# Performance work log

Hardware: AMD Instinct MI355X
Metric: run time of the kernel (lower is better)

Reference implementation:

```python
import jax, jax.numpy as jnp
import numpy as np
from jax import lax

IMG_SIZE = 1024.0  # nominal image dimension for generating plausible coords
IOU_THRESHOLD = 0.5


def box_iou(a, b):
    # a: (N,4), b: (M,4) in (x1,y1,x2,y2); returns (N,M) IoU
    area_a = (a[:, 2] - a[:, 0]) * (a[:, 3] - a[:, 1])
    area_b = (b[:, 2] - b[:, 0]) * (b[:, 3] - b[:, 1])
    lt = jnp.maximum(a[:, None, :2], b[None, :, :2])
    rb = jnp.minimum(a[:, None, 2:], b[None, :, 2:])
    wh = jnp.clip(rb - lt, 0.0)
    inter = wh[..., 0] * wh[..., 1]
    return inter / (area_a[:, None] + area_b[None, :] - inter)


def apply_deltas_to_locations(deltas, locations, stride):
    # Faithful to fcos_apply_deltas_to_locations: clip deltas at 0,
    # un-normalize by stride, subtract/add around the center location.
    d = jnp.clip(deltas, 0.0)  # (N,4) = (l, t, r, b)
    xc, yc = locations[:, 0], locations[:, 1]
    x1 = xc - stride * d[:, 0]
    y1 = yc - stride * d[:, 1]
    x2 = xc + stride * d[:, 2]
    y2 = yc + stride * d[:, 3]
    return jnp.stack([x1, y1, x2, y2], axis=1)


def nms_keep(boxes, scores, iou_threshold):
    # Greedy NMS, equivalent to the sequential reference loop:
    # process boxes in decreasing score order; a box survives if it is not
    # suppressed (IoU > thr) by any earlier surviving box.
    n = boxes.shape[0]
    order = jnp.argsort(-scores)  # descending score order
    b = boxes[order]
    iou = box_iou(b, b)  # (N,N), memory-bound pairwise compare
    idx = jnp.arange(n)

    def body(i, keep):
        suppress = (iou[i] > iou_threshold) & (idx > i) & keep[i]
        return keep & ~suppress

    keep_sorted = lax.fori_loop(0, n, body, jnp.ones((n,), dtype=bool))
    # scatter keep mask back to original ordering
    keep_orig = jnp.zeros((n,), dtype=bool).at[order].set(keep_sorted)
    return keep_orig, order, keep_sorted


def setup_inputs() -> dict:
    key = jax.random.key(0)
    k1, k2, k3, k4 = jax.random.split(key, 4)
    N = 8192
    deltas = jax.random.uniform(k1, (N, 4), dtype=jnp.float32) * 8.0  # stride-normalized LTRB
    locations = jax.random.uniform(k2, (N, 2), dtype=jnp.float32) * IMG_SIZE
    scores = jax.random.uniform(k3, (N,), dtype=jnp.float32)
    class_ids = jax.random.randint(k4, (N,), 0, 80, dtype=jnp.int32)
    return {"deltas": deltas, "locations": locations, "scores": scores,
            "class_ids": class_ids, "stride": 8}


def reference(deltas, locations, scores, class_ids, stride):
    # 1) LTRB delta decode (fcos_apply_deltas_to_locations)
    boxes = apply_deltas_to_locations(deltas, locations, stride)
    # 2) class-specific NMS (class_spec_nms): offset boxes per class so that
    #    boxes of different classes never overlap, then run plain NMS.
    max_coordinate = boxes.max()
    offsets = class_ids.astype(boxes.dtype) * (max_coordinate + 1.0)
    boxes_for_nms = boxes + offsets[:, None]
    keep_orig, order, keep_sorted = nms_keep(boxes_for_nms, scores, IOU_THRESHOLD)
    # boxes: decoded boxes; keep_orig: NMS survival mask (original order);
    # order: score-descending permutation (kept indices = order[keep_sorted])
    return boxes, keep_orig, order
```

## Files before the change

kernel.cpp:

```cpp
#include <hip/hip_runtime.h>

typedef unsigned long long u64;
typedef unsigned int u32;

#define NBOX 8192
#define NW64 128
#define NCLASS 80
#define NCMAX 256
#define CHKCAP 256
#define NS 32
#define SLICE 256
#define NBLK 32
#define RANKB (NS * NBLK)
#define K2GRID (RANKB + 1 + NCLASS)
#define K3GRID (NBLK + 1)

__device__ __forceinline__ u32 f32_mono(float f) {
  u32 u = __float_as_uint(f);
  return (u & 0x80000000u) ? ~u : (u | 0x80000000u);
}
__device__ __forceinline__ float mono_f32(u32 u) {
  u32 b = (u & 0x80000000u) ? (u ^ 0x80000000u) : ~u;
  return __uint_as_float(b);
}
__device__ __forceinline__ u64 readlane64(u64 v, int l) {
  u32 lo = __builtin_amdgcn_readlane((u32)v, l);
  u32 hi = __builtin_amdgcn_readlane((u32)(v >> 32), l);
  return ((u64)hi << 32) | (u64)lo;
}
__device__ __forceinline__ u32 reduce_bmax(const u32* __restrict__ bmax, int t) {
  u32 bm = bmax[t & 31];
#pragma unroll
  for (int off = 16; off > 0; off >>= 1) {
    u32 o = __shfl_xor(bm, off);
    bm = (bm > o) ? bm : o;
  }
  return bm;
}


__global__ __launch_bounds__(256) void decode_kernel(
    const float4* __restrict__ deltas, const float2* __restrict__ locs,
    const int* __restrict__ stride_p, float4* __restrict__ boxes_out,
    u32* __restrict__ bmax) {
  const int t = threadIdx.x;
  const int i = blockIdx.x * 256 + t;
  __shared__ u32 wmax[4];
  float s = (float)(*stride_p);
  float4 d = deltas[i];
  d.x = fmaxf(d.x, 0.f); d.y = fmaxf(d.y, 0.f);
  d.z = fmaxf(d.z, 0.f); d.w = fmaxf(d.w, 0.f);
  float2 c = locs[i];
  float4 bb;
  bb.x = c.x - s * d.x;
  bb.y = c.y - s * d.y;
  bb.z = c.x + s * d.z;
  bb.w = c.y + s * d.w;
  boxes_out[i] = bb;
  float m = fmaxf(fmaxf(bb.x, bb.y), fmaxf(bb.z, bb.w));
  u32 u = f32_mono(m);
#pragma unroll
  for (int off = 32; off > 0; off >>= 1) {
    u32 o = __shfl_xor(u, off);
    u = (u > o) ? u : o;
  }
  if ((t & 63) == 0) wmax[t >> 6] = u;
  __syncthreads();
  if (t == 0) {
    u32 m0 = wmax[0] > wmax[1] ? wmax[0] : wmax[1];
    u32 m1 = wmax[2] > wmax[3] ? wmax[2] : wmax[3];
    bmax[blockIdx.x] = m0 > m1 ? m0 : m1;
  }
}

__global__ __launch_bounds__(256) void rank_nms_kernel(
    const float* __restrict__ scores, const int* __restrict__ class_ids,
    const float4* __restrict__ boxes, const u32* __restrict__ bmax,
    float* __restrict__ keep_out, int* __restrict__ flag,
    int* __restrict__ rankp) {
  const int t = threadIdx.x;
  const int b = blockIdx.x;

  if (b < RANKB) {
    const int bi = b & 31;
    const int slice = b >> 5;
    const int i = bi * 256 + t;
    __shared__ u32 st[SLICE];
    st[t] = f32_mono(scores[slice * 256 + t]);
    __syncthreads();
    u32 mi = f32_mono(scores[i]);
    int tp = i - slice * 256;
    int cnt = 0;
#pragma unroll 8
    for (int p = 0; p < SLICE; ++p) {
      u32 mj = st[p];
      bool less = (mj > mi) || (mj == mi && p < tp);
      cnt += less ? 1 : 0;
    }
    rankp[slice * NBOX + i] = cnt;
    return;
  }

  if (b == RANKB) {
    __shared__ float4 bxA[CHKCAP], bxB[CHKCAP];
    __shared__ int clsA[CHKCAP], clsB[CHKCAP];
    __shared__ int hist[NCLASS];
    __shared__ int na, nb, hitf;
    if (t == 0) { na = 0; nb = 0; hitf = 0; }
    if (t < NCLASS) hist[t] = 0;
    __syncthreads();
    float M = mono_f32(reduce_bmax(bmax, t));
    float thrA = M - 65.0f;
    for (int base = 0; base < NBOX; base += 256) {
      int i = base + t;
      float4 bb = boxes[i];
      int cls = class_ids[i];
      atomicAdd(&hist[cls], 1);
      if (bb.z > thrA && bb.w > thrA) {
        int p = atomicAdd(&na, 1);
        if (p < CHKCAP) { bxA[p] = bb; clsA[p] = cls; }
      }
      if (bb.x < 1.0f && bb.y < 1.0f) {
        int p = atomicAdd(&nb, 1);
        if (p < CHKCAP) { bxB[p] = bb; clsB[p] = cls; }
      }
    }
    __syncthreads();
    if (t < NCLASS && hist[t] > NCMAX) atomicOr(&hitf, 1);
    int NA = na < CHKCAP ? na : CHKCAP;
    int NB = nb < CHKCAP ? nb : CHKCAP;
    bool hit = (t == 0) && (na > CHKCAP || nb > CHKCAP);
    for (int pr = t; pr < NA * NB; pr += 256) {
      int a = pr / NB, b2 = pr % NB;
      if (clsB[b2] != clsA[a] + 1) continue;
      float offa = (float)clsA[a] * (M + 1.0f);
      float offb = (float)clsB[b2] * (M + 1.0f);
      float4 A = bxA[a], Bb = bxB[b2];
      A.x += offa; A.y += offa; A.z += offa; A.w += offa;
      Bb.x += offb; Bb.y += offb; Bb.z += offb; Bb.w += offb;
      float ltx = fmaxf(A.x, Bb.x), lty = fmaxf(A.y, Bb.y);
      float rbx = fminf(A.z, Bb.z), rby = fminf(A.w, Bb.w);
      float ww = fmaxf(rbx - ltx, 0.f), hh = fmaxf(rby - lty, 0.f);
      float inter = ww * hh;
      float aa = (A.z - A.x) * (A.w - A.y);
      float ab = (Bb.z - Bb.x) * (Bb.w - Bb.y);
      float iou = inter / (aa + ab - inter);
      if (iou > 0.4f) hit = true;
    }
    if (hit) atomicOr(&hitf, 1);
    __syncthreads();
    if (t == 0) *flag = hitf;
    return;
  }

  const int c = b - (RANKB + 1);
  __shared__ u64 ck[NCMAX];
  __shared__ u32 slist[NCMAX];
  __shared__ float4 bx[NCMAX];
  __shared__ u64 smask[NCMAX][4];
  __shared__ int cnt_s;
  if (t == 0) cnt_s = 0;
  __syncthreads();

  float M = mono_f32(reduce_bmax(bmax, t));
  float off = (float)c * (M + 1.0f);

  {
    const int4* ci4 = (const int4*)class_ids;
    const float4* sc4 = (const float4*)scores;
#pragma unroll
    for (int it = 0; it < 8; ++it) {
      int g = it * 256 + t;
      int4 c4 = ci4[g];
      float4 s4 = sc4[g];
      int e = g * 4;
      if (c4.x == c) { int p = atomicAdd(&cnt_s, 1); if (p < NCMAX) ck[p] = ((u64)(~f32_mono(s4.x)) << 32) | (u32)(e); }
      if (c4.y == c) { int p = atomicAdd(&cnt_s, 1); if (p < NCMAX) ck[p] = ((u64)(~f32_mono(s4.y)) << 32) | (u32)(e + 1); }
      if (c4.z == c) { int p = atomicAdd(&cnt_s, 1); if (p < NCMAX) ck[p] = ((u64)(~f32_mono(s4.z)) << 32) | (u32)(e + 2); }
      if (c4.w == c) { int p = atomicAdd(&cnt_s, 1); if (p < NCMAX) ck[p] = ((u64)(~f32_mono(s4.w)) << 32) | (u32)(e + 3); }
    }
  }
  __syncthreads();
  int nc = cnt_s;
  if (nc > NCMAX) return;

  if (t < nc) {
    u64 kme = ck[t];
    int r2 = 0;
    for (int p = 0; p < nc; ++p) r2 += (ck[p] < kme) ? 1 : 0;
    slist[r2] = (u32)kme;
  }
  __syncthreads();

  for (int k = t; k < nc; k += 256) {
    float4 bb = boxes[slist[k]];
    bb.x += off; bb.y += off; bb.z += off; bb.w += off;
    bx[k] = bb;
  }
  __syncthreads();

  {
    const int wv = t >> 6;
    const int lane = t & 63;
    const int nw = (nc + 63) >> 6;
    for (int i = wv; i < nc; i += 4) {
      float4 bi = bx[i];
      float area_i = (bi.z - bi.x) * (bi.w - bi.y);
      for (int w = 0; w < nw; ++w) {
        int j2 = w * 64 + lane;
        float4 bj = bx[j2 < NCMAX ? j2 : 0];
        float ltx = fmaxf(bi.x, bj.x), lty = fmaxf(bi.y, bj.y);
        float rbx = fminf(bi.z, bj.z), rby = fminf(bi.w, bj.w);
        float ww = fmaxf(rbx - ltx, 0.f), hh = fmaxf(rby - lty, 0.f);
        float inter = ww * hh;
        float area_j = (bj.z - bj.x) * (bj.w - bj.y);
        float iou = inter / (area_i + area_j - inter);
        bool p = (iou > 0.5f) && (j2 > i) && (j2 < nc);
        u64 mm = __ballot(p);
        if (lane == 0) smask[i][w] = mm;
      }
    }
  }
  __syncthreads();
  if (t >= 64) return;

  u64 ma[4], mb[4], mc[4], md[4];
#pragma unroll
  for (int w = 0; w < 4; ++w) {
    ma[w] = smask[t][w];
    mb[w] = smask[64 + t][w];
    mc[w] = smask[128 + t][w];
    md[w] = smask[192 + t][w];
  }
  u64 R0 = 0, R1 = 0, R2 = 0, R3 = 0;
  u64 K0 = 0, K1 = 0, K2 = 0, K3 = 0;

#define SCAND(D, MD, RD, KD)                                                   \
  {                                                                            \
    int lim = nc - (D) * 64;                                                   \
    if (lim > 0) {                                                             \
      if (lim > 64) lim = 64;                                                  \
      for (int ii = 0; ii < lim; ++ii) {                                       \
        u64 kb = ((RD >> ii) & 1ull) ^ 1ull;                                   \
        KD |= kb << ii;                                                        \
        u64 sm2 = 0ull - kb;                                                   \
        R0 |= readlane64(MD[0], ii) & sm2;                                     \
        R1 |= readlane64(MD[1], ii) & sm2;                                     \
        R2 |= readlane64(MD[2], ii) & sm2;                                     \
        R3 |= readlane64(MD[3], ii) & sm2;                                     \
      }                                                                        \
    }                                                                          \
  }
  SCAND(0, ma, R0, K0)
  SCAND(1, mb, R1, K1)
  SCAND(2, mc, R2, K2)
  SCAND(3, md, R3, K3)
#undef SCAND

  u64 kk[4] = {K0, K1, K2, K3};
#pragma unroll
  for (int d = 0; d < 4; ++d) {
    int j = d * 64 + t;
    if (j < nc) keep_out[slist[j]] = ((kk[d] >> t) & 1ull) ? 1.0f : 0.0f;
  }
}

__global__ __launch_bounds__(256) void scatter_fallback_kernel(
    const int* __restrict__ class_ids, const float4* __restrict__ boxes,
    const u32* __restrict__ bmax, const int* __restrict__ rankp,
    float* __restrict__ order_out, float* __restrict__ keep_out,
    const int* __restrict__ flag) {
  const int t = threadIdx.x;
  const int bid = blockIdx.x;

  if (bid < NBLK) {
    int i = bid * 256 + t;
    int r = 0;
#pragma unroll
    for (int s2 = 0; s2 < NS; ++s2) r += rankp[s2 * NBOX + i];
    order_out[r] = (float)i;
    return;
  }

  if (*flag == 0) return;
  __shared__ u32 perm[NBOX];
  __shared__ u64 remv[NW64];
  for (int k = t; k < NW64; k += 256) remv[k] = 0;
  for (int i = t; i < NBOX; i += 256) {
    int r = 0;
#pragma unroll
    for (int s2 = 0; s2 < NS; ++s2) r += rankp[s2 * NBOX + i];
    perm[r] = (u32)i;
  }
  __syncthreads();
  float maxc = mono_f32(reduce_bmax(bmax, t));
  if (t < 64) {
    int lane = t;
    for (int ii = 0; ii < NBOX; ++ii) {
      if ((remv[ii >> 6] >> (ii & 63)) & 1ull) continue;
      u32 pi = perm[ii];
      float offi = (float)class_ids[pi] * (maxc + 1.0f);
      float4 bi = boxes[pi];
      bi.x += offi; bi.y += offi; bi.z += offi; bi.w += offi;
      float area_i = (bi.z - bi.x) * (bi.w - bi.y);
      for (int jb = ii + 1; jb < NBOX; jb += 64) {
        int j = jb + lane;
        bool p = false;
        if (j < NBOX) {
          u32 pj = perm[j];
          float offj = (float)class_ids[pj] * (maxc + 1.0f);
          float4 bj = boxes[pj];
          bj.x += offj; bj.y += offj; bj.z += offj; bj.w += offj;
          float ltx = fmaxf(bi.x, bj.x), lty = fmaxf(bi.y, bj.y);
          float rbx = fminf(bi.z, bj.z), rby = fminf(bi.w, bj.w);
          float ww = fmaxf(rbx - ltx, 0.f), hh = fmaxf(rby - lty, 0.f);
          float inter = ww * hh;
          float area_j = (bj.z - bj.x) * (bj.w - bj.y);
          float iou = inter / (area_i + area_j - inter);
          p = iou > 0.5f;
        }
        u64 m = __ballot(p);
        if (lane == 0 && m) {
          int w0 = jb >> 6, sh = jb & 63;
          remv[w0] |= (m << sh);
          if (sh && (w0 + 1) < NW64) remv[w0 + 1] |= (m >> (64 - sh));
        }
      }
    }
  }
  __syncthreads();
  for (int k = t; k < NBOX; k += 256)
    keep_out[perm[k]] = ((remv[k >> 6] >> (k & 63)) & 1ull) ? 0.0f : 1.0f;
}

extern "C" void kernel_launch(void* const* d_in, const int* in_sizes, int n_in,
                              void* d_out, int out_size, void* d_ws, size_t ws_size,
                              hipStream_t stream) {
  const float* deltas = (const float*)d_in[0];
  const float* locs = (const float*)d_in[1];
  const float* scores = (const float*)d_in[2];
  const int* class_ids = (const int*)d_in[3];
  const int* stride_p = (const int*)d_in[4];

  float* boxes_out = (float*)d_out;
  float* keep_out = (float*)d_out + (size_t)NBOX * 4;
  float* order_out = (float*)d_out + (size_t)NBOX * 5;

  u32* bmax = (u32*)((char*)d_ws + 64);
  int* flag = (int*)((char*)d_ws + 256);
  int* rankp = (int*)((char*)d_ws + 4096);

  decode_kernel<<<NBLK, 256, 0, stream>>>(
      (const float4*)deltas, (const float2*)locs, stride_p,
      (float4*)boxes_out, bmax);

  rank_nms_kernel<<<K2GRID, 256, 0, stream>>>(
      scores, class_ids, (const float4*)boxes_out, bmax, keep_out, flag,
      rankp);

  scatter_fallback_kernel<<<K3GRID, 256, 0, stream>>>(
      class_ids, (const float4*)boxes_out, bmax, rankp, order_out, keep_out,
      flag);
}
```

Baseline: 45.64 us.

## Reorder fused kernel blocks, union shared memory, move class histogram into decode

```diff
diff --git a/kernel.cpp b/kernel.cpp
--- a/kernel.cpp
+++ b/kernel.cpp
@@ -12,8 +12,9 @@
 #define SLICE 256
 #define NBLK 32
 #define RANKB (NS * NBLK)
-#define K2GRID (RANKB + 1 + NCLASS)
+#define K2GRID (NCLASS + 1 + RANKB)
 #define K3GRID (NBLK + 1)
+#define SMEMSZ 15616
 
 __device__ __forceinline__ u32 f32_mono(float f) {
   u32 u = __float_as_uint(f);
@@ -41,11 +42,14 @@
 
 __global__ __launch_bounds__(256) void decode_kernel(
     const float4* __restrict__ deltas, const float2* __restrict__ locs,
-    const int* __restrict__ stride_p, float4* __restrict__ boxes_out,
-    u32* __restrict__ bmax) {
+    const int* __restrict__ stride_p, const int* __restrict__ class_ids,
+    float4* __restrict__ boxes_out, u32* __restrict__ bmax,
+    int* __restrict__ ccpart) {
   const int t = threadIdx.x;
   const int i = blockIdx.x * 256 + t;
   __shared__ u32 wmax[4];
+  __shared__ int lhist[NCLASS];
+  if (t < NCLASS) lhist[t] = 0;
   float s = (float)(*stride_p);
   float4 d = deltas[i];
   d.x = fmaxf(d.x, 0.f); d.y = fmaxf(d.y, 0.f);
@@ -66,67 +70,177 @@
   }
   if ((t & 63) == 0) wmax[t >> 6] = u;
   __syncthreads();
+  atomicAdd(&lhist[class_ids[i]], 1);
   if (t == 0) {
     u32 m0 = wmax[0] > wmax[1] ? wmax[0] : wmax[1];
     u32 m1 = wmax[2] > wmax[3] ? wmax[2] : wmax[3];
     bmax[blockIdx.x] = m0 > m1 ? m0 : m1;
   }
+  __syncthreads();
+  if (t < NCLASS) ccpart[blockIdx.x * NCLASS + t] = lhist[t];
 }
 
 __global__ __launch_bounds__(256) void rank_nms_kernel(
     const float* __restrict__ scores, const int* __restrict__ class_ids,
     const float4* __restrict__ boxes, const u32* __restrict__ bmax,
-    float* __restrict__ keep_out, int* __restrict__ flag,
-    int* __restrict__ rankp) {
+    const int* __restrict__ ccpart, float* __restrict__ keep_out,
+    int* __restrict__ flag, int* __restrict__ rankp) {
   const int t = threadIdx.x;
-  const int b = blockIdx.x;
-
-  if (b < RANKB) {
-    const int bi = b & 31;
-    const int slice = b >> 5;
-    const int i = bi * 256 + t;
-    __shared__ u32 st[SLICE];
-    st[t] = f32_mono(scores[slice * 256 + t]);
-    __syncthreads();
-    u32 mi = f32_mono(scores[i]);
-    int tp = i - slice * 256;
-    int cnt = 0;
+  const int bid = blockIdx.x;
+  __shared__ __align__(16) char smem[SMEMSZ];
+
+  if (bid < NCLASS) {
+    const int c = bid;
+    u64* ck = (u64*)smem;
+    u32* slist = (u32*)(smem + 2048);
+    float4* bx = (float4*)(smem + 3072);
+    u64(*smask)[4] = (u64(*)[4])(smem + 7168);
+    int* cnt_s = (int*)(smem + 15360);
+    if (t == 0) *cnt_s = 0;
+    __syncthreads();
+
+    float M = mono_f32(reduce_bmax(bmax, t));
+    float off = (float)c * (M + 1.0f);
+
+    {
+      const int4* ci4 = (const int4*)class_ids;
+      const float4* sc4 = (const float4*)scores;
+#pragma unroll
+      for (int it = 0; it < 8; ++it) {
+        int g = it * 256 + t;
+        int4 c4 = ci4[g];
+        float4 s4 = sc4[g];
+        int e = g * 4;
+        if (c4.x == c) { int p = atomicAdd(cnt_s, 1); if (p < NCMAX) ck[p] = ((u64)(~f32_mono(s4.x)) << 32) | (u32)(e); }
+        if (c4.y == c) { int p = atomicAdd(cnt_s, 1); if (p < NCMAX) ck[p] = ((u64)(~f32_mono(s4.y)) << 32) | (u32)(e + 1); }
+        if (c4.z == c) { int p = atomicAdd(cnt_s, 1); if (p < NCMAX) ck[p] = ((u64)(~f32_mono(s4.z)) << 32) | (u32)(e + 2); }
+        if (c4.w == c) { int p = atomicAdd(cnt_s, 1); if (p < NCMAX) ck[p] = ((u64)(~f32_mono(s4.w)) << 32) | (u32)(e + 3); }
+      }
+    }
+    __syncthreads();
+    int nc = *cnt_s;
+    if (nc > NCMAX) return;
+
+    if (t < nc) {
+      u64 kme = ck[t];
+      int r2 = 0;
+      for (int p = 0; p < nc; ++p) r2 += (ck[p] < kme) ? 1 : 0;
+      slist[r2] = (u32)kme;
+    }
+    __syncthreads();
+
+    for (int k = t; k < nc; k += 256) {
+      float4 bb = boxes[slist[k]];
+      bb.x += off; bb.y += off; bb.z += off; bb.w += off;
+      bx[k] = bb;
+    }
+    __syncthreads();
+
+    {
+      const int wv = t >> 6;
+      const int lane = t & 63;
+      const int nw = (nc + 63) >> 6;
+      for (int i = wv; i < nc; i += 4) {
+        float4 bi = bx[i];
+        float area_i = (bi.z - bi.x) * (bi.w - bi.y);
+        for (int w = 0; w < nw; ++w) {
+          int j2 = w * 64 + lane;
+          float4 bj = bx[j2 < NCMAX ? j2 : 0];
+          float ltx = fmaxf(bi.x, bj.x), lty = fmaxf(bi.y, bj.y);
+          float rbx = fminf(bi.z, bj.z), rby = fminf(bi.w, bj.w);
+          float ww = fmaxf(rbx - ltx, 0.f), hh = fmaxf(rby - lty, 0.f);
+          float inter = ww * hh;
+          float area_j = (bj.z - bj.x) * (bj.w - bj.y);
+          float iou = inter / (area_i + area_j - inter);
+          bool p = (iou > 0.5f) && (j2 > i) && (j2 < nc);
+          u64 mm = __ballot(p);
+          if (lane == 0) smask[i][w] = mm;
+        }
+      }
+    }
+    __syncthreads();
+    if (t >= 64) return;
+
+    u64 ma[4], mb[4], mc[4], md[4];
+#pragma unroll
+    for (int w = 0; w < 4; ++w) {
+      ma[w] = smask[t][w];
+      mb[w] = smask[64 + t][w];
+      mc[w] = smask[128 + t][w];
+      md[w] = smask[192 + t][w];
+    }
+    u64 R0 = 0, R1 = 0, R2 = 0, R3 = 0;
+    u64 K0 = 0, K1 = 0, K2 = 0, K3 = 0;
+
+#define SCAND(D, MD, RD, KD)                                                   \
+  {                                                                            \
+    int lim = nc - (D) * 64;                                                   \
+    if (lim > 0) {                                                             \
+      if (lim > 64) lim = 64;                                                  \
+      for (int ii = 0; ii < lim; ++ii) {                                       \
+        u64 kb = ((RD >> ii) & 1ull) ^ 1ull;                                   \
+        KD |= kb << ii;                                                        \
+        u64 sm2 = 0ull - kb;                                                   \
+        R0 |= readlane64(MD[0], ii) & sm2;                                     \
+        R1 |= readlane64(MD[1], ii) & sm2;                                     \
+        R2 |= readlane64(MD[2], ii) & sm2;                                     \
+        R3 |= readlane64(MD[3], ii) & sm2;                                     \
+      }                                                                        \
+    }                                                                          \
+  }
+    SCAND(0, ma, R0, K0)
+    SCAND(1, mb, R1, K1)
+    SCAND(2, mc, R2, K2)
+    SCAND(3, md, R3, K3)
+#undef SCAND
+
+    u64 kk[4] = {K0, K1, K2, K3};
+#pragma unroll
+    for (int d = 0; d < 4; ++d) {
+      int j = d * 64 + t;
+      if (j < nc) keep_out[slist[j]] = ((kk[d] >> t) & 1ull) ? 1.0f : 0.0f;
+    }
+    return;
+  }
+
+  if (bid == NCLASS) {
+    float4* bxA = (float4*)smem;
+    float4* bxB = (float4*)(smem + 4096);
+    int* clsA = (int*)(smem + 8192);
+    int* clsB = (int*)(smem + 9216);
+    int* cnts = (int*)(smem + 10240);
+    if (t == 0) { cnts[0] = 0; cnts[1] = 0; cnts[2] = 0; }
+    __syncthreads();
+    if (t < NCLASS) {
+      int ssum = 0;
 #pragma unroll 8
-    for (int p = 0; p < SLICE; ++p) {
-      u32 mj = st[p];
-      bool less = (mj > mi) || (mj == mi && p < tp);
-      cnt += less ? 1 : 0;
-    }
-    rankp[slice * NBOX + i] = cnt;
-    return;
-  }
-
-  if (b == RANKB) {
-    __shared__ float4 bxA[CHKCAP], bxB[CHKCAP];
-    __shared__ int clsA[CHKCAP], clsB[CHKCAP];
-    __shared__ int hist[NCLASS];
-    __shared__ int na, nb, hitf;
-    if (t == 0) { na = 0; nb = 0; hitf = 0; }
-    if (t < NCLASS) hist[t] = 0;
-    __syncthreads();
+      for (int b2 = 0; b2 < NBLK; ++b2) ssum += ccpart[b2 * NCLASS + t];
+      if (ssum > NCMAX) atomicOr(&cnts[2], 1);
+    }
     float M = mono_f32(reduce_bmax(bmax, t));
     float thrA = M - 65.0f;
-    for (int base = 0; base < NBOX; base += 256) {
-      int i = base + t;
-      float4 bb = boxes[i];
-      int cls = class_ids[i];
-      atomicAdd(&hist[cls], 1);
-      if (bb.z > thrA && bb.w > thrA) {
-        int p = atomicAdd(&na, 1);
-        if (p < CHKCAP) { bxA[p] = bb; clsA[p] = cls; }
+#pragma unroll
+    for (int it = 0; it < 4; ++it) {
+      float4 v[8];
+      int cl[8];
+#pragma unroll
+      for (int r = 0; r < 8; ++r) v[r] = boxes[it * 2048 + r * 256 + t];
+#pragma unroll
+      for (int r = 0; r < 8; ++r) cl[r] = class_ids[it * 2048 + r * 256 + t];
+#pragma unroll
+      for (int r = 0; r < 8; ++r) {
+        if (v[r].z > thrA && v[r].w > thrA) {
+          int p = atomicAdd(&cnts[0], 1);
+          if (p < CHKCAP) { bxA[p] = v[r]; clsA[p] = cl[r]; }
+        }
+        if (v[r].x < 1.0f && v[r].y < 1.0f) {
+          int p = atomicAdd(&cnts[1], 1);
+          if (p < CHKCAP) { bxB[p] = v[r]; clsB[p] = cl[r]; }
+        }
       }
-      if (bb.x < 1.0f && bb.y < 1.0f) {
-        int p = atomicAdd(&nb, 1);
-        if (p < CHKCAP) { bxB[p] = bb; clsB[p] = cls; }
-      }
-    }
-    __syncthreads();
-    if (t < NCLASS && hist[t] > NCMAX) atomicOr(&hitf, 1);
+    }
+    __syncthreads();
+    int na = cnts[0], nb = cnts[1];
     int NA = na < CHKCAP ? na : CHKCAP;
     int NB = nb < CHKCAP ? nb : CHKCAP;
     bool hit = (t == 0) && (na > CHKCAP || nb > CHKCAP);
@@ -147,122 +261,29 @@
       float iou = inter / (aa + ab - inter);
       if (iou > 0.4f) hit = true;
     }
-    if (hit) atomicOr(&hitf, 1);
-    __syncthreads();
-    if (t == 0) *flag = hitf;
+    if (hit) atomicOr(&cnts[2], 1);
+    __syncthreads();
+    if (t == 0) *flag = cnts[2];
     return;
   }
 
-  const int c = b - (RANKB + 1);
-  __shared__ u64 ck[NCMAX];
-  __shared__ u32 slist[NCMAX];
-  __shared__ float4 bx[NCMAX];
-  __shared__ u64 smask[NCMAX][4];
-  __shared__ int cnt_s;
-  if (t == 0) cnt_s = 0;
-  __syncthreads();
-
-  float M = mono_f32(reduce_bmax(bmax, t));
-  float off = (float)c * (M + 1.0f);
-
-  {
-    const int4* ci4 = (const int4*)class_ids;
-    const float4* sc4 = (const float4*)scores;
-#pragma unroll
-    for (int it = 0; it < 8; ++it) {
-      int g = it * 256 + t;
-      int4 c4 = ci4[g];
-      float4 s4 = sc4[g];
-      int e = g * 4;
-      if (c4.x == c) { int p = atomicAdd(&cnt_s, 1); if (p < NCMAX) ck[p] = ((u64)(~f32_mono(s4.x)) << 32) | (u32)(e); }
-      if (c4.y == c) { int p = atomicAdd(&cnt_s, 1); if (p < NCMAX) ck[p] = ((u64)(~f32_mono(s4.y)) << 32) | (u32)(e + 1); }
-      if (c4.z == c) { int p = atomicAdd(&cnt_s, 1); if (p < NCMAX) ck[p] = ((u64)(~f32_mono(s4.z)) << 32) | (u32)(e + 2); }
-      if (c4.w == c) { int p = atomicAdd(&cnt_s, 1); if (p < NCMAX) ck[p] = ((u64)(~f32_mono(s4.w)) << 32) | (u32)(e + 3); }
-    }
-  }
-  __syncthreads();
-  int nc = cnt_s;
-  if (nc > NCMAX) return;
-
-  if (t < nc) {
-    u64 kme = ck[t];
-    int r2 = 0;
-    for (int p = 0; p < nc; ++p) r2 += (ck[p] < kme) ? 1 : 0;
-    slist[r2] = (u32)kme;
-  }
-  __syncthreads();
-
-  for (int k = t; k < nc; k += 256) {
-    float4 bb = boxes[slist[k]];
-    bb.x += off; bb.y += off; bb.z += off; bb.w += off;
-    bx[k] = bb;
-  }
-  __syncthreads();
-
-  {
-    const int wv = t >> 6;
-    const int lane = t & 63;
-    const int nw = (nc + 63) >> 6;
-    for (int i = wv; i < nc; i += 4) {
-      float4 bi = bx[i];
-      float area_i = (bi.z - bi.x) * (bi.w - bi.y);
-      for (int w = 0; w < nw; ++w) {
-        int j2 = w * 64 + lane;
-        float4 bj = bx[j2 < NCMAX ? j2 : 0];
-        float ltx = fmaxf(bi.x, bj.x), lty = fmaxf(bi.y, bj.y);
-        float rbx = fminf(bi.z, bj.z), rby = fminf(bi.w, bj.w);
-        float ww = fmaxf(rbx - ltx, 0.f), hh = fmaxf(rby - lty, 0.f);
-        float inter = ww * hh;
-        float area_j = (bj.z - bj.x) * (bj.w - bj.y);
-        float iou = inter / (area_i + area_j - inter);
-        bool p = (iou > 0.5f) && (j2 > i) && (j2 < nc);
-        u64 mm = __ballot(p);
-        if (lane == 0) smask[i][w] = mm;
-      }
-    }
-  }
-  __syncthreads();
-  if (t >= 64) return;
-
-  u64 ma[4], mb[4], mc[4], md[4];
-#pragma unroll
-  for (int w = 0; w < 4; ++w) {
-    ma[w] = smask[t][w];
-    mb[w] = smask[64 + t][w];
-    mc[w] = smask[128 + t][w];
-    md[w] = smask[192 + t][w];
-  }
-  u64 R0 = 0, R1 = 0, R2 = 0, R3 = 0;
-  u64 K0 = 0, K1 = 0, K2 = 0, K3 = 0;
-
-#define SCAND(D, MD, RD, KD)                                                   \
-  {                                                                            \
-    int lim = nc - (D) * 64;                                                   \
-    if (lim > 0) {                                                             \
-      if (lim > 64) lim = 64;                                                  \
-      for (int ii = 0; ii < lim; ++ii) {                                       \
-        u64 kb = ((RD >> ii) & 1ull) ^ 1ull;                                   \
-        KD |= kb << ii;                                                        \
-        u64 sm2 = 0ull - kb;                                                   \
-        R0 |= readlane64(MD[0], ii) & sm2;                                     \
-        R1 |= readlane64(MD[1], ii) & sm2;                                     \
-        R2 |= readlane64(MD[2], ii) & sm2;                                     \
-        R3 |= readlane64(MD[3], ii) & sm2;                                     \
-      }                                                                        \
-    }                                                                          \
-  }
-  SCAND(0, ma, R0, K0)
-  SCAND(1, mb, R1, K1)
-  SCAND(2, mc, R2, K2)
-  SCAND(3, md, R3, K3)
-#undef SCAND
-
-  u64 kk[4] = {K0, K1, K2, K3};
-#pragma unroll
-  for (int d = 0; d < 4; ++d) {
-    int j = d * 64 + t;
-    if (j < nc) keep_out[slist[j]] = ((kk[d] >> t) & 1ull) ? 1.0f : 0.0f;
-  }
+  const int rb = bid - (NCLASS + 1);
+  const int bi = rb & 31;
+  const int slice = rb >> 5;
+  const int i = bi * 256 + t;
+  u32* st = (u32*)smem;
+  st[t] = f32_mono(scores[slice * 256 + t]);
+  __syncthreads();
+  u32 mi = f32_mono(scores[i]);
+  int tp = i - slice * 256;
+  int cnt = 0;
+#pragma unroll 8
+  for (int p = 0; p < SLICE; ++p) {
+    u32 mj = st[p];
+    bool less = (mj > mi) || (mj == mi && p < tp);
+    cnt += less ? 1 : 0;
+  }
+  rankp[slice * NBOX + i] = cnt;
 }
 
 __global__ __launch_bounds__(256) void scatter_fallback_kernel(
@@ -348,15 +369,16 @@
 
   u32* bmax = (u32*)((char*)d_ws + 64);
   int* flag = (int*)((char*)d_ws + 256);
-  int* rankp = (int*)((char*)d_ws + 4096);
+  int* ccpart = (int*)((char*)d_ws + 512);
+  int* rankp = (int*)((char*)d_ws + 16384);
 
   decode_kernel<<<NBLK, 256, 0, stream>>>(
-      (const float4*)deltas, (const float2*)locs, stride_p,
-      (float4*)boxes_out, bmax);
+      (const float4*)deltas, (const float2*)locs, stride_p, class_ids,
+      (float4*)boxes_out, bmax, ccpart);
 
   rank_nms_kernel<<<K2GRID, 256, 0, stream>>>(
-      scores, class_ids, (const float4*)boxes_out, bmax, keep_out, flag,
-      rankp);
+      scores, class_ids, (const float4*)boxes_out, bmax, ccpart, keep_out,
+      flag, rankp);
 
   scatter_fallback_kernel<<<K3GRID, 256, 0, stream>>>(
       class_ids, (const float4*)boxes_out, bmax, rankp, order_out, keep_out,
```

Result: faster. 42.36 us, median of 2 (-7.2%).
